# Performance work log

Measured on AMD Instinct MI355X. Metric: run time of the kernel, lower is better.

The kernel has to match this reference:

```python
import jax, jax.numpy as jnp
import numpy as np

EMB = 2048
NH = 16
HD = EMB // NH  # 128

def setup_inputs() -> dict:
    key = jax.random.key(0)
    kx, kw1, kw2 = jax.random.split(key, 3)
    T = 4096
    x = jax.random.normal(kx, (T, EMB), dtype=jnp.float32)
    lim_in = 1.0 / np.sqrt(EMB)
    # input_proj: Linear(EMB, 3*EMB, use_bias=False), weight shape (out, in)
    W_in = jax.random.uniform(kw1, (3 * EMB, EMB), minval=-lim_in, maxval=lim_in, dtype=jnp.float32)
    W_out = jax.random.uniform(kw2, (EMB, EMB), minval=-lim_in, maxval=lim_in, dtype=jnp.float32)
    return {"x": x, "W_in": W_in, "W_out": W_out}

def reference(x, W_in, W_out):
    T = x.shape[0]
    norm = 1.0 / np.sqrt(HD)
    qkv = x @ W_in.T                         # [T, 3E]
    Q, K, V = jnp.split(qkv, 3, axis=-1)     # each [T, E]
    Q = Q.reshape(T, NH, HD).transpose(1, 0, 2)  # [nh, T, hd]
    K = K.reshape(T, NH, HD).transpose(1, 0, 2)
    V = V.reshape(T, NH, HD).transpose(1, 0, 2)
    A = jnp.einsum('htd,hsd->hts', Q, K) * norm  # [nh, T, T]
    mask = jnp.tri(T, dtype=bool)                # causal: keep lower triangle
    A = jnp.where(mask, A, -jnp.inf)
    P = jax.nn.softmax(A, axis=-1)
    y = jnp.einsum('hts,hsd->htd', P, V)         # [nh, T, hd]
    y = y.transpose(1, 0, 2).reshape(T, EMB)     # concat heads
    return y @ W_out.T
```

## Files before the change

kernel.cpp:

```cpp
#include <hip/hip_runtime.h>
#include <hip/hip_bf16.h>
#include <cstddef>


typedef __attribute__((ext_vector_type(8))) short short8;
typedef __attribute__((ext_vector_type(4))) float f32x4;

#define MFMA16(a, b, c) __builtin_amdgcn_mfma_f32_16x16x32_bf16((a), (b), (c), 0, 0, 0)

#define GLOAD_LDS16(gptr, lptr)                                                          \
  __builtin_amdgcn_global_load_lds((const __attribute__((address_space(1))) void*)(gptr), \
                                   (__attribute__((address_space(3))) void*)(lptr), 16, 0, 0)

#define PSWZ(q) ((((q) & 7) ^ ((q) >> 3)) << 3)

__device__ __forceinline__ short f2bf(float f) {
  __hip_bfloat16 h = __float2bfloat16(f);
  return *reinterpret_cast<short*>(&h);
}

__device__ __forceinline__ void storeC(float* p, float v) { *p = v; }
__device__ __forceinline__ void storeC(short* p, float v) { *p = f2bf(v); }

__global__ void cvt_bf16(const float* __restrict__ in, short* __restrict__ out,
                         long n, float scale, long scaleN) {
  long i = ((long)blockIdx.x * 256 + threadIdx.x) * 8;
  if (i >= n) return;
  float s = (i < scaleN) ? scale : 1.0f;
  f32x4 a = *(const f32x4*)(in + i);
  f32x4 b = *(const f32x4*)(in + i + 4);
  short8 o;
  o[0] = f2bf(a[0] * s); o[1] = f2bf(a[1] * s); o[2] = f2bf(a[2] * s); o[3] = f2bf(a[3] * s);
  o[4] = f2bf(b[0] * s); o[5] = f2bf(b[1] * s); o[6] = f2bf(b[2] * s); o[7] = f2bf(b[3] * s);
  *(short8*)(out + i) = o;
}

template <typename CT>
__global__ __launch_bounds__(256, 2)
void gemm_bt(const short* __restrict__ A, const short* __restrict__ B,
             CT* __restrict__ C, int M, int N, int K) {
  __shared__ short As[128 * 32];
  __shared__ short Bs[128 * 32];
  const int tid = threadIdx.x;
  const int wave = tid >> 6, lane = tid & 63;
  const int g = lane >> 4, fr = lane & 15;
  const int wr = (wave >> 1) * 64, wc = (wave & 1) * 64;
  const int bm = blockIdx.y * 128, bn = blockIdx.x * 128;

  f32x4 acc[4][4] = {};

  for (int k0 = 0; k0 < K; k0 += 32) {
    __syncthreads();
#pragma unroll
    for (int i = 0; i < 2; ++i) {
      int Ci = i * 256 + tid;
      int row = Ci >> 2, c = Ci & 3;
      int sc = c ^ (row & 3);
      GLOAD_LDS16(A + (size_t)(bm + row) * K + k0 + sc * 8, As + Ci * 8);
      GLOAD_LDS16(B + (size_t)(bn + row) * K + k0 + sc * 8, Bs + Ci * 8);
    }
    __syncthreads();

    short8 af[4], bfr[4];
#pragma unroll
    for (int m = 0; m < 4; ++m) {
      int row = wr + m * 16 + fr;
      int off = (g * 8) ^ ((row & 3) * 8);
      af[m] = *(const short8*)(As + row * 32 + off);
    }
#pragma unroll
    for (int n = 0; n < 4; ++n) {
      int row = wc + n * 16 + fr;
      int off = (g * 8) ^ ((row & 3) * 8);
      bfr[n] = *(const short8*)(Bs + row * 32 + off);
    }
#pragma unroll
    for (int m = 0; m < 4; ++m)
#pragma unroll
      for (int n = 0; n < 4; ++n)
        acc[m][n] = MFMA16(af[m], bfr[n], acc[m][n]);
  }

#pragma unroll
  for (int m = 0; m < 4; ++m) {
#pragma unroll
    for (int r = 0; r < 4; ++r) {
      size_t row = (size_t)(bm + wr + m * 16 + g * 4 + r);
      CT* cp = C + row * N + bn + wc + fr;
#pragma unroll
      for (int n = 0; n < 4; ++n)
        storeC(cp + n * 16, acc[m][n][r]);
    }
  }
}

__global__ __launch_bounds__(256, 4)
void vtrans(const short* __restrict__ qkv, short* __restrict__ vtg) {
  __shared__ short L[128 * 64];
  const int tid = threadIdx.x;
  const int tb = blockIdx.x * 64;
  const int h = blockIdx.y;
#pragma unroll
  for (int i = 0; i < 4; ++i) {
    int Ci = i * 256 + tid, tok = Ci >> 4, c = Ci & 15, f0 = c * 8;
    short8 v = *(const short8*)(qkv + (size_t)(tb + tok) * 6144 + 4096 + h * 128 + f0);
#pragma unroll
    for (int j = 0; j < 8; ++j) {
      int f = f0 + j;
      L[f * 64 + (tok ^ ((((f & 7) ^ ((f >> 3) & 7)) << 3)))] = v[j];
    }
  }
  __syncthreads();
  const int f = tid >> 1, half = (tid & 1) * 32;
  const int s_in = ((f & 7) ^ ((f >> 3) & 7)) << 3;
  const int s_out = (f & 7) << 3;
#pragma unroll
  for (int j2 = 0; j2 < 4; ++j2) {
    int t0 = half + j2 * 8;
    short8 v = *(const short8*)(&L[f * 64 + (t0 ^ s_in)]);
    *(short8*)(vtg + (size_t)(h * 128 + f) * 4096 + tb + (t0 ^ s_out)) = v;
  }
}

__global__ __launch_bounds__(256, 2)
void attn_fwd(const short* __restrict__ qkv, const short* __restrict__ vtg,
              short* __restrict__ y) {
  __shared__ short Ks[2][64 * 128];
  __shared__ short Vt[2][128 * 64];
  __shared__ short Ps[4][32 * 64];
  const int tid = threadIdx.x;
  const int wave = tid >> 6, lane = tid & 63;
  const int g = lane >> 4, fr = lane & 15;

  const int wgid = blockIdx.x;
  const int slot = wgid >> 3;
  const int h = ((wgid & 7) << 1) | (slot >> 4);
  const int pair = slot & 15;

  short* Pw = Ps[wave];

  short8 onesf;
#pragma unroll
  for (int j = 0; j < 8; ++j) onesf[j] = (short)0x3F80;

#pragma unroll 1
  for (int phase = 0; phase < 2; ++phase) {
    const int xb = phase ? (31 - pair) : pair;
    const int qw = xb * 128 + wave * 32;
    const int ntiles = 2 * xb + 2;

    short8 qf[2][4];
#pragma unroll
    for (int mi = 0; mi < 2; ++mi) {
      const short* Qp = qkv + (size_t)(qw + mi * 16 + fr) * 6144 + h * 128;
#pragma unroll
      for (int kk = 0; kk < 4; ++kk)
        qf[mi][kk] = *(const short8*)(Qp + kk * 32 + g * 8);
    }
    f32x4 oacc[2][8] = {};
    f32x4 lacc[2] = {};

#pragma unroll
    for (int i = 0; i < 4; ++i) {
      int Ci = i * 256 + tid, key = Ci >> 4, c = Ci & 15, sc = c ^ (key & 7);
      GLOAD_LDS16(qkv + (size_t)key * 6144 + 2048 + h * 128 + sc * 8, &Ks[0][Ci * 8]);
    }
#pragma unroll
    for (int i = 0; i < 4; ++i) {
      int Ci = i * 256 + tid, feat = Ci >> 3, ko = (Ci & 7) * 8;
      GLOAD_LDS16(vtg + (size_t)(h * 128 + feat) * 4096 + ko, &Vt[0][Ci * 8]);
    }
    __syncthreads();

#pragma unroll 1
    for (int t = 0; t < ntiles; ++t) {
      const int kv0 = t * 64;
      const int cur = t & 1;

      if (t + 1 < ntiles) {
#pragma unroll
        for (int i = 0; i < 4; ++i) {
          int Ci = i * 256 + tid, key = Ci >> 4, c = Ci & 15, sc = c ^ (key & 7);
          GLOAD_LDS16(qkv + (size_t)(kv0 + 64 + key) * 6144 + 2048 + h * 128 + sc * 8,
                      &Ks[cur ^ 1][Ci * 8]);
        }
#pragma unroll
        for (int i = 0; i < 4; ++i) {
          int Ci = i * 256 + tid, feat = Ci >> 3, ko = (Ci & 7) * 8;
          GLOAD_LDS16(vtg + (size_t)(h * 128 + feat) * 4096 + kv0 + 64 + ko,
                      &Vt[cur ^ 1][Ci * 8]);
        }
      }

      f32x4 s[2][4] = {};
      __builtin_amdgcn_s_setprio(1);
#pragma unroll
      for (int nf = 0; nf < 4; ++nf) {
        const int key = nf * 16 + fr;
#pragma unroll
        for (int kk = 0; kk < 4; ++kk) {
          int off = (kk * 32 + g * 8) ^ ((key & 7) * 8);
          short8 kfrag = *(const short8*)(&Ks[cur][key * 128 + off]);
          s[0][nf] = MFMA16(qf[0][kk], kfrag, s[0][nf]);
          s[1][nf] = MFMA16(qf[1][kk], kfrag, s[1][nf]);
        }
      }
      __builtin_amdgcn_s_setprio(0);

      if (t >= ntiles - 2) {
#pragma unroll
        for (int mi = 0; mi < 2; ++mi)
#pragma unroll
          for (int nf = 0; nf < 4; ++nf) {
            const int keyg = kv0 + nf * 16 + fr;
#pragma unroll
            for (int r = 0; r < 4; ++r) {
              const int q2 = mi * 16 + g * 4 + r;
              float p = (keyg <= qw + q2) ? __builtin_amdgcn_exp2f(s[mi][nf][r]) : 0.f;
              Pw[q2 * 64 + ((nf * 16 + fr) ^ PSWZ(q2))] = f2bf(p);
            }
          }
      } else {
#pragma unroll
        for (int mi = 0; mi < 2; ++mi)
#pragma unroll
          for (int nf = 0; nf < 4; ++nf)
#pragma unroll
            for (int r = 0; r < 4; ++r) {
              const int q2 = mi * 16 + g * 4 + r;
              Pw[q2 * 64 + ((nf * 16 + fr) ^ PSWZ(q2))] =
                  f2bf(__builtin_amdgcn_exp2f(s[mi][nf][r]));
            }
      }

      __builtin_amdgcn_s_setprio(1);
#pragma unroll
      for (int kk = 0; kk < 2; ++kk) {
        const int rb = kk * 32 + g * 8;
        short8 pf0 = *(const short8*)(&Pw[fr * 64 + (rb ^ PSWZ(fr))]);
        short8 pf1 = *(const short8*)(&Pw[(16 + fr) * 64 + (rb ^ PSWZ(16 + fr))]);
        lacc[0] = MFMA16(pf0, onesf, lacc[0]);
        lacc[1] = MFMA16(pf1, onesf, lacc[1]);
#pragma unroll
        for (int nf = 0; nf < 8; ++nf) {
          int f = nf * 16 + fr;
          short8 vf = *(const short8*)(&Vt[cur][f * 64 + (rb ^ ((f & 7) * 8))]);
          oacc[0][nf] = MFMA16(pf0, vf, oacc[0][nf]);
          oacc[1][nf] = MFMA16(pf1, vf, oacc[1][nf]);
        }
      }
      __builtin_amdgcn_s_setprio(0);

      __syncthreads();
    }

#pragma unroll
    for (int mi = 0; mi < 2; ++mi)
#pragma unroll
      for (int r = 0; r < 4; ++r) {
        float inv = 1.0f / lacc[mi][r];
        size_t row = (size_t)(qw + mi * 16 + g * 4 + r);
#pragma unroll
        for (int nf = 0; nf < 8; ++nf)
          y[row * 2048 + h * 128 + nf * 16 + fr] = f2bf(oacc[mi][nf][r] * inv);
      }
  }
}

extern "C" void kernel_launch(void* const* d_in, const int* in_sizes, int n_in,
                              void* d_out, int out_size, void* d_ws, size_t ws_size,
                              hipStream_t stream) {
  const float* x    = (const float*)d_in[0];
  const float* Win  = (const float*)d_in[1];
  const float* Wout = (const float*)d_in[2];
  float* out = (float*)d_out;

  char* ws = (char*)d_ws;
  short* xb    = (short*)(ws);
  short* yb    = (short*)(ws);
  short* Winb  = (short*)(ws + 16777216);
  short* vtg   = (short*)(ws + 16777216);
  short* Woutb = (short*)(ws + 41943040);
  short* qkv   = (short*)(ws + 50331648);

  const float qscale = 0.08838834764831845f * 1.4426950408889634f;

  cvt_bf16<<<4096, 256, 0, stream>>>(x, xb, 8388608L, 1.0f, 0L);
  cvt_bf16<<<6144, 256, 0, stream>>>(Win, Winb, 12582912L, qscale, 4194304L);
  cvt_bf16<<<2048, 256, 0, stream>>>(Wout, Woutb, 4194304L, 1.0f, 0L);

  gemm_bt<short><<<dim3(48, 32), 256, 0, stream>>>(xb, Winb, qkv, 4096, 6144, 2048);

  vtrans<<<dim3(64, 16), 256, 0, stream>>>(qkv, vtg);

  attn_fwd<<<256, 256, 0, stream>>>(qkv, vtg, yb);

  gemm_bt<float><<<dim3(16, 32), 256, 0, stream>>>(yb, Woutb, out, 4096, 2048, 2048);
}
```

Before: 341.1 us.

## Deepen GEMM K-tile, split attention blocks per query tile, single-buffer V

The GEMM now stages 64-wide K slices with an 8-way XOR swizzle and asks for 4 blocks per CU, which halves the number of barrier-bounded iterations. The attention kernel stops having each block handle a pair of query tiles one after the other. It launches 512 blocks with one query tile each, mapped so that each XCD keeps its own heads. V^T becomes single-buffered and is loaded at the start of each iteration behind an extra barrier, which frees LDS. Each wave also skips QK/PV work on tiles that are fully masked. The costs are reduced overlap between V loads and compute, an extra sync per tile, and possible register spills from the tighter launch bounds.

```diff
diff --git a/kernel.cpp b/kernel.cpp
--- a/kernel.cpp
+++ b/kernel.cpp
@@ -36,11 +36,11 @@
 }
 
 template <typename CT>
-__global__ __launch_bounds__(256, 2)
+__global__ __launch_bounds__(256, 4)
 void gemm_bt(const short* __restrict__ A, const short* __restrict__ B,
              CT* __restrict__ C, int M, int N, int K) {
-  __shared__ short As[128 * 32];
-  __shared__ short Bs[128 * 32];
+  __shared__ short As[128 * 64];
+  __shared__ short Bs[128 * 64];
   const int tid = threadIdx.x;
   const int wave = tid >> 6, lane = tid & 63;
   const int g = lane >> 4, fr = lane & 15;
@@ -49,36 +49,39 @@
 
   f32x4 acc[4][4] = {};
 
-  for (int k0 = 0; k0 < K; k0 += 32) {
+  for (int k0 = 0; k0 < K; k0 += 64) {
     __syncthreads();
 #pragma unroll
-    for (int i = 0; i < 2; ++i) {
+    for (int i = 0; i < 4; ++i) {
       int Ci = i * 256 + tid;
-      int row = Ci >> 2, c = Ci & 3;
-      int sc = c ^ (row & 3);
+      int row = Ci >> 3, c = Ci & 7;
+      int sc = c ^ (row & 7);
       GLOAD_LDS16(A + (size_t)(bm + row) * K + k0 + sc * 8, As + Ci * 8);
       GLOAD_LDS16(B + (size_t)(bn + row) * K + k0 + sc * 8, Bs + Ci * 8);
     }
     __syncthreads();
 
-    short8 af[4], bfr[4];
-#pragma unroll
-    for (int m = 0; m < 4; ++m) {
-      int row = wr + m * 16 + fr;
-      int off = (g * 8) ^ ((row & 3) * 8);
-      af[m] = *(const short8*)(As + row * 32 + off);
-    }
-#pragma unroll
-    for (int n = 0; n < 4; ++n) {
-      int row = wc + n * 16 + fr;
-      int off = (g * 8) ^ ((row & 3) * 8);
-      bfr[n] = *(const short8*)(Bs + row * 32 + off);
-    }
-#pragma unroll
-    for (int m = 0; m < 4; ++m)
-#pragma unroll
-      for (int n = 0; n < 4; ++n)
-        acc[m][n] = MFMA16(af[m], bfr[n], acc[m][n]);
+#pragma unroll
+    for (int kk = 0; kk < 2; ++kk) {
+      short8 af[4], bfr[4];
+#pragma unroll
+      for (int m = 0; m < 4; ++m) {
+        int row = wr + m * 16 + fr;
+        int off = (kk * 32 + g * 8) ^ ((row & 7) * 8);
+        af[m] = *(const short8*)(As + row * 64 + off);
+      }
+#pragma unroll
+      for (int n = 0; n < 4; ++n) {
+        int row = wc + n * 16 + fr;
+        int off = (kk * 32 + g * 8) ^ ((row & 7) * 8);
+        bfr[n] = *(const short8*)(Bs + row * 64 + off);
+      }
+#pragma unroll
+      for (int m = 0; m < 4; ++m)
+#pragma unroll
+        for (int n = 0; n < 4; ++n)
+          acc[m][n] = MFMA16(af[m], bfr[n], acc[m][n]);
+    }
   }
 
 #pragma unroll
@@ -126,16 +129,19 @@
 void attn_fwd(const short* __restrict__ qkv, const short* __restrict__ vtg,
               short* __restrict__ y) {
   __shared__ short Ks[2][64 * 128];
-  __shared__ short Vt[2][128 * 64];
+  __shared__ short Vt[128 * 64];
   __shared__ short Ps[4][32 * 64];
   const int tid = threadIdx.x;
   const int wave = tid >> 6, lane = tid & 63;
   const int g = lane >> 4, fr = lane & 15;
 
   const int wgid = blockIdx.x;
-  const int slot = wgid >> 3;
-  const int h = ((wgid & 7) << 1) | (slot >> 4);
-  const int pair = slot & 15;
+  const int xcd = wgid & 7, mid = (wgid >> 3) & 31, slot = wgid >> 8;
+  const int h = (xcd << 1) | (mid & 1);
+  const int xq = mid >> 1;
+  const int x = slot ? xq : 31 - xq;
+  const int qw = x * 128 + wave * 32;
+  const int ntiles = 2 * x + 2;
 
   short* Pw = Ps[wave];
 
@@ -143,55 +149,53 @@
 #pragma unroll
   for (int j = 0; j < 8; ++j) onesf[j] = (short)0x3F80;
 
+  short8 qf[2][4];
+#pragma unroll
+  for (int mi = 0; mi < 2; ++mi) {
+    const short* Qp = qkv + (size_t)(qw + mi * 16 + fr) * 6144 + h * 128;
+#pragma unroll
+    for (int kk = 0; kk < 4; ++kk)
+      qf[mi][kk] = *(const short8*)(Qp + kk * 32 + g * 8);
+  }
+  f32x4 oacc[2][8] = {};
+  f32x4 lacc[2] = {};
+
+#pragma unroll
+  for (int i = 0; i < 4; ++i) {
+    int Ci = i * 256 + tid, key = Ci >> 4, c = Ci & 15, sc = c ^ (key & 7);
+    GLOAD_LDS16(qkv + (size_t)key * 6144 + 2048 + h * 128 + sc * 8, &Ks[0][Ci * 8]);
+  }
+#pragma unroll
+  for (int i = 0; i < 4; ++i) {
+    int Ci = i * 256 + tid, feat = Ci >> 3, ko = (Ci & 7) * 8;
+    GLOAD_LDS16(vtg + (size_t)(h * 128 + feat) * 4096 + ko, &Vt[Ci * 8]);
+  }
+  __syncthreads();
+
 #pragma unroll 1
-  for (int phase = 0; phase < 2; ++phase) {
-    const int xb = phase ? (31 - pair) : pair;
-    const int qw = xb * 128 + wave * 32;
-    const int ntiles = 2 * xb + 2;
-
-    short8 qf[2][4];
-#pragma unroll
-    for (int mi = 0; mi < 2; ++mi) {
-      const short* Qp = qkv + (size_t)(qw + mi * 16 + fr) * 6144 + h * 128;
-#pragma unroll
-      for (int kk = 0; kk < 4; ++kk)
-        qf[mi][kk] = *(const short8*)(Qp + kk * 32 + g * 8);
-    }
-    f32x4 oacc[2][8] = {};
-    f32x4 lacc[2] = {};
-
-#pragma unroll
-    for (int i = 0; i < 4; ++i) {
-      int Ci = i * 256 + tid, key = Ci >> 4, c = Ci & 15, sc = c ^ (key & 7);
-      GLOAD_LDS16(qkv + (size_t)key * 6144 + 2048 + h * 128 + sc * 8, &Ks[0][Ci * 8]);
-    }
-#pragma unroll
-    for (int i = 0; i < 4; ++i) {
-      int Ci = i * 256 + tid, feat = Ci >> 3, ko = (Ci & 7) * 8;
-      GLOAD_LDS16(vtg + (size_t)(h * 128 + feat) * 4096 + ko, &Vt[0][Ci * 8]);
-    }
-    __syncthreads();
-
-#pragma unroll 1
-    for (int t = 0; t < ntiles; ++t) {
-      const int kv0 = t * 64;
-      const int cur = t & 1;
-
-      if (t + 1 < ntiles) {
-#pragma unroll
-        for (int i = 0; i < 4; ++i) {
-          int Ci = i * 256 + tid, key = Ci >> 4, c = Ci & 15, sc = c ^ (key & 7);
-          GLOAD_LDS16(qkv + (size_t)(kv0 + 64 + key) * 6144 + 2048 + h * 128 + sc * 8,
-                      &Ks[cur ^ 1][Ci * 8]);
-        }
-#pragma unroll
-        for (int i = 0; i < 4; ++i) {
-          int Ci = i * 256 + tid, feat = Ci >> 3, ko = (Ci & 7) * 8;
-          GLOAD_LDS16(vtg + (size_t)(h * 128 + feat) * 4096 + kv0 + 64 + ko,
-                      &Vt[cur ^ 1][Ci * 8]);
-        }
-      }
-
+  for (int t = 0; t < ntiles; ++t) {
+    const int kv0 = t * 64;
+    const int cur = t & 1;
+
+    if (t > 0) {
+#pragma unroll
+      for (int i = 0; i < 4; ++i) {
+        int Ci = i * 256 + tid, feat = Ci >> 3, ko = (Ci & 7) * 8;
+        GLOAD_LDS16(vtg + (size_t)(h * 128 + feat) * 4096 + kv0 + ko, &Vt[Ci * 8]);
+      }
+    }
+    if (t + 1 < ntiles) {
+#pragma unroll
+      for (int i = 0; i < 4; ++i) {
+        int Ci = i * 256 + tid, key = Ci >> 4, c = Ci & 15, sc = c ^ (key & 7);
+        GLOAD_LDS16(qkv + (size_t)(kv0 + 64 + key) * 6144 + 2048 + h * 128 + sc * 8,
+                    &Ks[cur ^ 1][Ci * 8]);
+      }
+    }
+
+    const bool active = (kv0 <= qw + 31);
+
+    if (active) {
       f32x4 s[2][4] = {};
       __builtin_amdgcn_s_setprio(1);
 #pragma unroll
@@ -232,7 +236,11 @@
                   f2bf(__builtin_amdgcn_exp2f(s[mi][nf][r]));
             }
       }
-
+    }
+
+    __syncthreads();
+
+    if (active) {
       __builtin_amdgcn_s_setprio(1);
 #pragma unroll
       for (int kk = 0; kk < 2; ++kk) {
@@ -244,27 +252,27 @@
 #pragma unroll
         for (int nf = 0; nf < 8; ++nf) {
           int f = nf * 16 + fr;
-          short8 vf = *(const short8*)(&Vt[cur][f * 64 + (rb ^ ((f & 7) * 8))]);
+          short8 vf = *(const short8*)(&Vt[f * 64 + (rb ^ ((f & 7) * 8))]);
           oacc[0][nf] = MFMA16(pf0, vf, oacc[0][nf]);
           oacc[1][nf] = MFMA16(pf1, vf, oacc[1][nf]);
         }
       }
       __builtin_amdgcn_s_setprio(0);
-
-      __syncthreads();
-    }
-
-#pragma unroll
-    for (int mi = 0; mi < 2; ++mi)
-#pragma unroll
-      for (int r = 0; r < 4; ++r) {
-        float inv = 1.0f / lacc[mi][r];
-        size_t row = (size_t)(qw + mi * 16 + g * 4 + r);
-#pragma unroll
-        for (int nf = 0; nf < 8; ++nf)
-          y[row * 2048 + h * 128 + nf * 16 + fr] = f2bf(oacc[mi][nf][r] * inv);
-      }
-  }
+    }
+
+    __syncthreads();
+  }
+
+#pragma unroll
+  for (int mi = 0; mi < 2; ++mi)
+#pragma unroll
+    for (int r = 0; r < 4; ++r) {
+      float inv = 1.0f / lacc[mi][r];
+      size_t row = (size_t)(qw + mi * 16 + g * 4 + r);
+#pragma unroll
+      for (int nf = 0; nf < 8; ++nf)
+        y[row * 2048 + h * 128 + nf * 16 + fr] = f2bf(oacc[mi][nf][r] * inv);
+    }
 }
 
 extern "C" void kernel_launch(void* const* d_in, const int* in_sizes, int n_in,
@@ -293,7 +301,7 @@
 
   vtrans<<<dim3(64, 16), 256, 0, stream>>>(qkv, vtg);
 
-  attn_fwd<<<256, 256, 0, stream>>>(qkv, vtg, yb);
+  attn_fwd<<<512, 256, 0, stream>>>(qkv, vtg, yb);
 
   gemm_bt<float><<<dim3(16, 32), 256, 0, stream>>>(yb, Woutb, out, 4096, 2048, 2048);
 }
```

New measurement: 284.2 us. 16.7% less time.
